# Kernel tuning notes

Hardware: AMD Instinct MI355X
Metric: run time of the kernel (lower is better)

## Reference

```python
import jax, jax.numpy as jnp
import numpy as np

N_NODES = 100000
N_EDGES = 1600000
D_FEAT = 48
K = 10
ALPHA = 0.1


def setup_inputs() -> dict:
    key = jax.random.key(0)
    k1, k2, k3 = jax.random.split(key, 3)
    x = jax.random.normal(k1, (N_NODES, D_FEAT), dtype=jnp.float32)
    edge_index = jax.random.randint(k2, (2, N_EDGES), 0, N_NODES, dtype=jnp.int64)
    edge_weight = jax.random.uniform(k3, (N_EDGES,), dtype=jnp.float32)
    return {"x": x, "edge_index": edge_index, "edge_weight": edge_weight}


def reference(x, edge_index, edge_weight):
    row, col = edge_index[0], edge_index[1]
    # degree-weighted normalization: w_ij / sum_j w_ij
    deg_w = jax.ops.segment_sum(edge_weight, row, num_segments=N_NODES)
    norm = edge_weight / (deg_w[row] + 1e-10)  # [E]

    def step(h, _):
        # gather h at source-of-message (col), scale, scatter-add to row
        msg = jax.ops.segment_sum(norm[:, None] * h[col], row, num_segments=N_NODES)
        h_new = (1.0 - ALPHA) * msg + ALPHA * x
        return h_new, None

    h, _ = jax.lax.scan(step, x, None, length=K)
    return h
```

## Files before the change

kernel.cpp:

```cpp
#include <hip/hip_runtime.h>
#include <hip/hip_fp16.h>

#define N_NODES 100000
#define N_EDGES 1600000
#define K_ITER 10

#define TPN 6
#define NPB 32
#define PAD 4

#define NBUCK 391
#define BROWS 256
#define BSTRIDE 4608
#define BK_TB 512
#define BK_EPT 16
#define BK_SEG (BK_TB * BK_EPT)
#define BK_NB ((N_EDGES + BK_SEG - 1) / BK_SEG)

#define NPART 16

typedef unsigned int u32;
typedef unsigned long long u64;

__global__ __launch_bounds__(BK_TB) void k_bucket(const int* __restrict__ row,
        const int* __restrict__ col, const float* __restrict__ w,
        u32* __restrict__ bcursor, u64* __restrict__ bedge, int E) {
    __shared__ u32 hcnt[NBUCK], sbase[NBUCK];
    int t = threadIdx.x;
    for (int b = t; b < NBUCK; b += BK_TB) hcnt[b] = 0;
    __syncthreads();
    int i0 = blockIdx.x * BK_SEG + t;
#pragma unroll
    for (int k = 0; k < BK_EPT; ++k) {
        int i = i0 + k * BK_TB;
        if (i < E) atomicAdd(&hcnt[((u32)row[i]) >> 8], 1u);
    }
    __syncthreads();
    for (int b = t; b < NBUCK; b += BK_TB) {
        u32 c = hcnt[b];
        sbase[b] = c ? atomicAdd(&bcursor[b], c) : 0u;
        hcnt[b] = 0;
    }
    __syncthreads();
#pragma unroll
    for (int k = 0; k < BK_EPT; ++k) {
        int i = i0 + k * BK_TB;
        if (i < E) {
            u32 r = (u32)row[i];
            u32 b = r >> 8;
            u32 rk = atomicAdd(&hcnt[b], 1u);
            u32 idx = sbase[b] + rk;
            if (idx < BSTRIDE)
                bedge[(u64)b * BSTRIDE + idx] =
                    ((u64)(r & 255u) << 32) | ((u64)(u32)col[i] << 15) |
                    (u64)(__float_as_uint(w[i]) >> 17);
        }
    }
}

__global__ __launch_bounds__(BROWS) void k_buildA(const u32* __restrict__ bcursor,
        const u64* __restrict__ bedge, uint4* __restrict__ cnt16,
        u32* __restrict__ bsum) {
    __shared__ u32 cnt[NPART * BROWS];
    __shared__ u32 sh[BROWS];
    int b = blockIdx.x, t = threadIdx.x;
#pragma unroll
    for (int k = 0; k < NPART; ++k) cnt[k * BROWS + t] = 0;
    __syncthreads();
    u32 cb = bcursor[b];
    if (cb > BSTRIDE) cb = BSTRIDE;
    const u64* be = bedge + (u64)b * BSTRIDE;
    for (u32 j = t; j < cb; j += BROWS) {
        u64 e = be[j];
        u32 r = (u32)(e >> 32) & 255u;
        u32 p = ((u32)e) >> 28;
        atomicAdd(&cnt[p * BROWS + r], 1u);
    }
    __syncthreads();
    u32 c[NPART], tot = 0;
#pragma unroll
    for (int p = 0; p < NPART; ++p) { c[p] = cnt[p * BROWS + t]; tot += c[p]; }
    uint4 pk;
    pk.x = c[0] | (c[1] << 8) | (c[2] << 16) | (c[3] << 24);
    pk.y = c[4] | (c[5] << 8) | (c[6] << 16) | (c[7] << 24);
    pk.z = c[8] | (c[9] << 8) | (c[10] << 16) | (c[11] << 24);
    pk.w = c[12] | (c[13] << 8) | (c[14] << 16) | (c[15] << 24);
    cnt16[b * BROWS + t] = pk;
    sh[t] = (tot + PAD - 1) & ~(u32)(PAD - 1);
    __syncthreads();
    for (int off = 128; off > 0; off >>= 1) {
        if (t < off) sh[t] += sh[t + off];
        __syncthreads();
    }
    if (t == 0) bsum[b] = sh[0];
}

__global__ void k_scanbk(const u32* __restrict__ bsum, u32* __restrict__ bbase,
                         int* __restrict__ rowptr) {
    __shared__ u32 sh[512];
    int t = threadIdx.x;
    u32 v = (t < NBUCK) ? bsum[t] : 0;
    sh[t] = v;
    __syncthreads();
    for (int off = 1; off < 512; off <<= 1) {
        u32 u = (t >= off) ? sh[t - off] : 0;
        __syncthreads();
        sh[t] += u;
        __syncthreads();
    }
    if (t < NBUCK) bbase[t] = sh[t] - v;
    if (t == NBUCK - 1) rowptr[N_NODES] = (int)sh[t];
}

__global__ __launch_bounds__(BROWS) void k_buildB(const u32* __restrict__ bcursor,
        const u64* __restrict__ bedge, const uint4* __restrict__ cnt16,
        const u32* __restrict__ bbase, int* __restrict__ rowptr,
        u32* __restrict__ epack, float* __restrict__ scale) {
    __shared__ u32 sh[BROWS];
    __shared__ u32 run[BROWS * NPART];
    __shared__ float swsum[BROWS];
    int b = blockIdx.x, t = threadIdx.x;
    uint4 pk = cnt16[b * BROWS + t];
    u32 c[NPART];
    c[0] = pk.x & 255u; c[1] = (pk.x >> 8) & 255u; c[2] = (pk.x >> 16) & 255u; c[3] = pk.x >> 24;
    c[4] = pk.y & 255u; c[5] = (pk.y >> 8) & 255u; c[6] = (pk.y >> 16) & 255u; c[7] = pk.y >> 24;
    c[8] = pk.z & 255u; c[9] = (pk.z >> 8) & 255u; c[10] = (pk.z >> 16) & 255u; c[11] = pk.z >> 24;
    c[12] = pk.w & 255u; c[13] = (pk.w >> 8) & 255u; c[14] = (pk.w >> 16) & 255u; c[15] = pk.w >> 24;
    u32 tot = 0;
#pragma unroll
    for (int p = 0; p < NPART; ++p) tot += c[p];
    u32 ptot = (tot + PAD - 1) & ~(u32)(PAD - 1);
    sh[t] = ptot;
    __syncthreads();
    for (int off = 1; off < BROWS; off <<= 1) {
        u32 u = (t >= off) ? sh[t - off] : 0;
        __syncthreads();
        sh[t] += u;
        __syncthreads();
    }
    u32 my = bbase[b] + sh[t] - ptot;
    int grow = b * BROWS + t;
    if (grow < N_NODES) rowptr[grow] = (int)my;
    u32 o = my;
#pragma unroll
    for (int p = 0; p < NPART; ++p) { run[t * NPART + p] = o; o += c[p]; }
    swsum[t] = 0.f;
    __syncthreads();
    u32 cb = bcursor[b];
    if (cb > BSTRIDE) cb = BSTRIDE;
    const u64* be = bedge + (u64)b * BSTRIDE;
    for (u32 j = t; j < cb; j += BROWS) {
        u64 e = be[j];
        u32 r = (u32)(e >> 32) & 255u;
        u32 pkv = (u32)e;
        u32 p = pkv >> 28;
        u32 pos = atomicAdd(&run[r * NPART + p], 1u);
        epack[pos] = pkv;
        atomicAdd(&swsum[r], __uint_as_float((pkv & 0x7fffu) << 17));
    }
    __syncthreads();
    if (grow < N_NODES) scale[grow] = 0.9f / (swsum[t] + 1e-10f);
}

__global__ void k_x2h(const float4* __restrict__ x, float4* __restrict__ x16) {
    int i = blockIdx.x * blockDim.x + threadIdx.x;
    int n = i / TPN, c = i % TPN;
    if (n >= N_NODES) return;
    float4 a = x[n * 12 + 2 * c], b = x[n * 12 + 2 * c + 1];
    float4 o;
    ((__half2*)&o)[0] = __floats2half2_rn(a.x, a.y);
    ((__half2*)&o)[1] = __floats2half2_rn(a.z, a.w);
    ((__half2*)&o)[2] = __floats2half2_rn(b.x, b.y);
    ((__half2*)&o)[3] = __floats2half2_rn(b.z, b.w);
    x16[(n << 3) + c] = o;
}

#define PFMA(UU, HV, AA, BB)                                                  \
    {                                                                         \
        float wv = __uint_as_float(((UU) & 0x7fffu) << 17) * sc;              \
        float2 f0 = __half22float2(*(__half2*)&HV.x);                         \
        float2 f1 = __half22float2(*(__half2*)&HV.y);                         \
        float2 f2 = __half22float2(*(__half2*)&HV.z);                         \
        float2 f3 = __half22float2(*(__half2*)&HV.w);                         \
        AA.x += wv * f0.x; AA.y += wv * f0.y; AA.z += wv * f1.x; AA.w += wv * f1.y; \
        BB.x += wv * f2.x; BB.y += wv * f2.y; BB.z += wv * f3.x; BB.w += wv * f3.y; \
    }

template <int LAST>
__global__ __launch_bounds__(192) void k_pull(const int* __restrict__ rowptr,
                                              const u32* __restrict__ epack,
                                              const float* __restrict__ scale,
                                              const float4* __restrict__ x,
                                              const float4* __restrict__ src16,
                                              void* __restrict__ dstv) {
    int node = blockIdx.x * NPB + threadIdx.x / TPN;
    int c = threadIdx.x % TPN;
    if (node >= N_NODES) return;
    int beg = rowptr[node], end = rowptr[node + 1];
    float sc = scale[node];
    float4 xa = x[node * 12 + 2 * c], xb = x[node * 12 + 2 * c + 1];
    float4 A0 = make_float4(0.1f * xa.x, 0.1f * xa.y, 0.1f * xa.z, 0.1f * xa.w);
    float4 B0 = make_float4(0.1f * xb.x, 0.1f * xb.y, 0.1f * xb.z, 0.1f * xb.w);
    float4 A1 = make_float4(0, 0, 0, 0), B1 = make_float4(0, 0, 0, 0);
    if (beg < end) {
        uint4 p = *(const uint4*)(epack + beg);
        float4 h0 = src16[((p.x >> 15) << 3) + c];
        float4 h1 = src16[((p.y >> 15) << 3) + c];
        float4 h2 = src16[((p.z >> 15) << 3) + c];
        float4 h3 = src16[((p.w >> 15) << 3) + c];
        for (int e = beg + 4; e < end; e += 4) {
            uint4 pn = *(const uint4*)(epack + e);
            float4 g0 = src16[((pn.x >> 15) << 3) + c];
            float4 g1 = src16[((pn.y >> 15) << 3) + c];
            float4 g2 = src16[((pn.z >> 15) << 3) + c];
            float4 g3 = src16[((pn.w >> 15) << 3) + c];
            PFMA(p.x, h0, A0, B0) PFMA(p.y, h1, A1, B1)
            PFMA(p.z, h2, A0, B0) PFMA(p.w, h3, A1, B1)
            p = pn; h0 = g0; h1 = g1; h2 = g2; h3 = g3;
        }
        PFMA(p.x, h0, A0, B0) PFMA(p.y, h1, A1, B1)
        PFMA(p.z, h2, A0, B0) PFMA(p.w, h3, A1, B1)
    }
    float4 RA = make_float4(A0.x + A1.x, A0.y + A1.y, A0.z + A1.z, A0.w + A1.w);
    float4 RB = make_float4(B0.x + B1.x, B0.y + B1.y, B0.z + B1.z, B0.w + B1.w);
    if (LAST) {
        float4* out = (float4*)dstv;
        out[node * 12 + 2 * c]     = RA;
        out[node * 12 + 2 * c + 1] = RB;
    } else {
        float4 o;
        ((__half2*)&o)[0] = __floats2half2_rn(RA.x, RA.y);
        ((__half2*)&o)[1] = __floats2half2_rn(RA.z, RA.w);
        ((__half2*)&o)[2] = __floats2half2_rn(RB.x, RB.y);
        ((__half2*)&o)[3] = __floats2half2_rn(RB.z, RB.w);
        ((float4*)dstv)[(node << 3) + c] = o;
    }
}

extern "C" void kernel_launch(void* const* d_in, const int* in_sizes, int n_in,
                              void* d_out, int out_size, void* d_ws, size_t ws_size,
                              hipStream_t stream) {
    const float* x  = (const float*)d_in[0];
    const int*   ei = (const int*)d_in[1];
    const float* w  = (const float*)d_in[2];
    const int E = in_sizes[2];
    const int* row = ei;
    const int* col = ei + E;

    char* ws = (char*)d_ws;
    int*    rowptr  = (int*)(ws);
    float*  scale   = (float*)(ws + 400032);
    u32*    bsum    = (u32*)(ws + 800032);
    u32*    bbase   = (u32*)(ws + 801600);
    u32*    bcursor = (u32*)(ws + 803168);
    uint4*  cnt16   = (uint4*)(ws + 804736);
    u32*    epack   = (u32*)(ws + 2406272);
    u64*    bedge   = (u64*)(ws + 10006336);
    float4* hB16    = (float4*)(ws + 14852352);
    float4* hA16    = (float4*)d_out;

    const int pgrid = N_NODES / NPB;
    const int xgrid = (N_NODES * TPN + 191) / 192;

    hipMemsetAsync(bcursor, 0, NBUCK * sizeof(u32), stream);
    hipMemsetAsync(epack, 0, (size_t)(N_EDGES + 3 * N_NODES + 16) * sizeof(u32), stream);
    k_bucket<<<BK_NB, BK_TB, 0, stream>>>(row, col, w, bcursor, bedge, E);
    k_buildA<<<NBUCK, BROWS, 0, stream>>>(bcursor, bedge, cnt16, bsum);
    k_scanbk<<<1, 512, 0, stream>>>(bsum, bbase, rowptr);
    k_buildB<<<NBUCK, BROWS, 0, stream>>>(bcursor, bedge, cnt16, bbase,
                                          rowptr, epack, scale);
    k_x2h  <<<xgrid, 192, 0, stream>>>((const float4*)x, hA16);

    float4* src = hA16;
    float4* dst = hB16;
    for (int k = 1; k <= K_ITER - 1; ++k) {
        k_pull<0><<<pgrid, NPB * TPN, 0, stream>>>(rowptr, epack, scale,
                                                   (const float4*)x, src, dst);
        float4* t = src; src = dst; dst = t;
    }
    k_pull<1><<<pgrid, NPB * TPN, 0, stream>>>(rowptr, epack, scale,
                                               (const float4*)x, src, d_out);
}
```

Measured before the change: 429.8 us.

## Sort nodes by degree bin so pull blocks have balanced edge counts

Adds a counting sort of nodes by in-degree (histogram, scan, fill) and builds permuted per-slot arrays for edge ranges, scale, node id and x. The pull kernel then iterates over slots, so threads within a wavefront handle rows of similar length, which reduces divergence and tail imbalance. The cost is four extra setup kernels plus an indirection on output writes, which are now scattered rather than coalesced.

```diff
diff --git a/kernel.cpp b/kernel.cpp
--- a/kernel.cpp
+++ b/kernel.cpp
@@ -18,6 +18,8 @@
 #define BK_NB ((N_EDGES + BK_SEG - 1) / BK_SEG)
 
 #define NPART 16
+
+#define DBINS 64
 
 typedef unsigned int u32;
 typedef unsigned long long u64;
@@ -162,6 +164,82 @@
     if (grow < N_NODES) scale[grow] = 0.9f / (swsum[t] + 1e-10f);
 }
 
+__global__ __launch_bounds__(BROWS) void k_dhist(const int* __restrict__ rowptr,
+                                                 u32* __restrict__ dhist) {
+    __shared__ u32 h[DBINS];
+    int t = threadIdx.x;
+    if (t < DBINS) h[t] = 0;
+    __syncthreads();
+    int n = blockIdx.x * BROWS + t;
+    if (n < N_NODES) {
+        int bin = min((rowptr[n + 1] - rowptr[n]) >> 2, DBINS - 1);
+        atomicAdd(&h[bin], 1u);
+    }
+    __syncthreads();
+    if (t < DBINS && h[t]) atomicAdd(&dhist[t * 16], h[t]);
+}
+
+__global__ void k_dscan(const u32* __restrict__ dhist, u32* __restrict__ dbase,
+                        u32* __restrict__ dcur) {
+    __shared__ u32 sh[DBINS];
+    int t = threadIdx.x;
+    u32 v = dhist[t * 16];
+    sh[t] = v;
+    __syncthreads();
+    for (int off = 1; off < DBINS; off <<= 1) {
+        u32 u = (t >= off) ? sh[t - off] : 0;
+        __syncthreads();
+        sh[t] += u;
+        __syncthreads();
+    }
+    dbase[t] = sh[t] - v;
+    for (int k = t; k < DBINS * 16; k += DBINS) dcur[k] = 0;
+}
+
+__global__ __launch_bounds__(BROWS) void k_dfill(const int* __restrict__ rowptr,
+        const u32* __restrict__ dbase, u32* __restrict__ dcur,
+        int* __restrict__ perm) {
+    __shared__ u32 h[DBINS];
+    __shared__ u32 sb[DBINS];
+    int t = threadIdx.x;
+    if (t < DBINS) h[t] = 0;
+    __syncthreads();
+    int n = blockIdx.x * BROWS + t;
+    int bin = 0;
+    if (n < N_NODES) {
+        bin = min((rowptr[n + 1] - rowptr[n]) >> 2, DBINS - 1);
+        atomicAdd(&h[bin], 1u);
+    }
+    __syncthreads();
+    if (t < DBINS) {
+        u32 c = h[t];
+        sb[t] = c ? atomicAdd(&dcur[t * 16], c) : 0u;
+        h[t] = 0;
+    }
+    __syncthreads();
+    if (n < N_NODES) {
+        u32 rk = atomicAdd(&h[bin], 1u);
+        perm[dbase[bin] + sb[bin] + rk] = n;
+    }
+}
+
+__global__ void k_pprep(const int* __restrict__ perm, const int* __restrict__ rowptr,
+        const float* __restrict__ scale, const float4* __restrict__ x,
+        u64* __restrict__ pbe, int* __restrict__ pnode,
+        float* __restrict__ pscale, float4* __restrict__ px) {
+    int i = blockIdx.x * blockDim.x + threadIdx.x;
+    int slot = i / TPN, c = i % TPN;
+    if (slot >= N_NODES) return;
+    int n = perm[slot];
+    px[slot * 12 + 2 * c]     = x[n * 12 + 2 * c];
+    px[slot * 12 + 2 * c + 1] = x[n * 12 + 2 * c + 1];
+    if (c == 0) {
+        pbe[slot]   = ((u64)(u32)rowptr[n] << 32) | (u32)rowptr[n + 1];
+        pnode[slot] = n;
+        pscale[slot] = scale[n];
+    }
+}
+
 __global__ void k_x2h(const float4* __restrict__ x, float4* __restrict__ x16) {
     int i = blockIdx.x * blockDim.x + threadIdx.x;
     int n = i / TPN, c = i % TPN;
@@ -187,18 +265,20 @@
     }
 
 template <int LAST>
-__global__ __launch_bounds__(192) void k_pull(const int* __restrict__ rowptr,
+__global__ __launch_bounds__(192) void k_pull(const u64* __restrict__ pbe,
+                                              const int* __restrict__ pnode,
+                                              const float* __restrict__ pscale,
+                                              const float4* __restrict__ px,
                                               const u32* __restrict__ epack,
-                                              const float* __restrict__ scale,
-                                              const float4* __restrict__ x,
                                               const float4* __restrict__ src16,
                                               void* __restrict__ dstv) {
-    int node = blockIdx.x * NPB + threadIdx.x / TPN;
+    int slot = blockIdx.x * NPB + threadIdx.x / TPN;
     int c = threadIdx.x % TPN;
-    if (node >= N_NODES) return;
-    int beg = rowptr[node], end = rowptr[node + 1];
-    float sc = scale[node];
-    float4 xa = x[node * 12 + 2 * c], xb = x[node * 12 + 2 * c + 1];
+    if (slot >= N_NODES) return;
+    u64 be = pbe[slot];
+    int beg = (int)(be >> 32), end = (int)(u32)be;
+    float sc = pscale[slot];
+    float4 xa = px[slot * 12 + 2 * c], xb = px[slot * 12 + 2 * c + 1];
     float4 A0 = make_float4(0.1f * xa.x, 0.1f * xa.y, 0.1f * xa.z, 0.1f * xa.w);
     float4 B0 = make_float4(0.1f * xb.x, 0.1f * xb.y, 0.1f * xb.z, 0.1f * xb.w);
     float4 A1 = make_float4(0, 0, 0, 0), B1 = make_float4(0, 0, 0, 0);
@@ -223,6 +303,7 @@
     }
     float4 RA = make_float4(A0.x + A1.x, A0.y + A1.y, A0.z + A1.z, A0.w + A1.w);
     float4 RB = make_float4(B0.x + B1.x, B0.y + B1.y, B0.z + B1.z, B0.w + B1.w);
+    int node = pnode[slot];
     if (LAST) {
         float4* out = (float4*)dstv;
         out[node * 12 + 2 * c]     = RA;
@@ -257,27 +338,42 @@
     u32*    epack   = (u32*)(ws + 2406272);
     u64*    bedge   = (u64*)(ws + 10006336);
     float4* hB16    = (float4*)(ws + 14852352);
+    int*    perm    = (int*)(ws + 27652352);
+    u32*    dhist   = (u32*)(ws + 28052352);
+    u32*    dbase   = (u32*)(ws + 28056448);
+    u32*    dcur    = (u32*)(ws + 28056704);
+    u64*    pbe     = (u64*)(ws + 28060800);
+    int*    pnode   = (int*)(ws + 28860800);
+    float*  pscale  = (float*)(ws + 29260800);
+    float4* px      = (float4*)(ws + 29660800);
     float4* hA16    = (float4*)d_out;
 
     const int pgrid = N_NODES / NPB;
     const int xgrid = (N_NODES * TPN + 191) / 192;
+    const int ngrid = (N_NODES + BROWS - 1) / BROWS;
 
     hipMemsetAsync(bcursor, 0, NBUCK * sizeof(u32), stream);
+    hipMemsetAsync(dhist, 0, DBINS * 16 * sizeof(u32), stream);
     hipMemsetAsync(epack, 0, (size_t)(N_EDGES + 3 * N_NODES + 16) * sizeof(u32), stream);
     k_bucket<<<BK_NB, BK_TB, 0, stream>>>(row, col, w, bcursor, bedge, E);
     k_buildA<<<NBUCK, BROWS, 0, stream>>>(bcursor, bedge, cnt16, bsum);
     k_scanbk<<<1, 512, 0, stream>>>(bsum, bbase, rowptr);
     k_buildB<<<NBUCK, BROWS, 0, stream>>>(bcursor, bedge, cnt16, bbase,
                                           rowptr, epack, scale);
+    k_dhist<<<ngrid, BROWS, 0, stream>>>(rowptr, dhist);
+    k_dscan<<<1, DBINS, 0, stream>>>(dhist, dbase, dcur);
+    k_dfill<<<ngrid, BROWS, 0, stream>>>(rowptr, dbase, dcur, perm);
+    k_pprep<<<xgrid, 192, 0, stream>>>(perm, rowptr, scale, (const float4*)x,
+                                       pbe, pnode, pscale, px);
     k_x2h  <<<xgrid, 192, 0, stream>>>((const float4*)x, hA16);
 
     float4* src = hA16;
     float4* dst = hB16;
     for (int k = 1; k <= K_ITER - 1; ++k) {
-        k_pull<0><<<pgrid, NPB * TPN, 0, stream>>>(rowptr, epack, scale,
-                                                   (const float4*)x, src, dst);
+        k_pull<0><<<pgrid, NPB * TPN, 0, stream>>>(pbe, pnode, pscale, px,
+                                                   epack, src, dst);
         float4* t = src; src = dst; dst = t;
     }
-    k_pull<1><<<pgrid, NPB * TPN, 0, stream>>>(rowptr, epack, scale,
-                                               (const float4*)x, src, d_out);
-}
+    k_pull<1><<<pgrid, NPB * TPN, 0, stream>>>(pbe, pnode, pscale, px,
+                                               epack, src, d_out);
+}
```

New measurement: 495.5 us. +15.3%, slower.
